# Kernel optimization log

Hardware: AMD Instinct MI355X
Metric: run time of the kernel (lower is better)

The kernel has to match this reference:

```python
import jax, jax.numpy as jnp
import numpy as np

B, T, D = 4, 1024, 1024
H = 16
DH = D // H            # head dim (attention_dim/num_heads)
FF = 4096
EPS = 1e-6             # allennlp LayerNorm eps
NEG = jnp.finfo(jnp.float32).min


def _layer_norm(x, g, b):
    # allennlp LayerNorm: (x - mean) / (unbiased_std + eps) * gamma + beta
    mean = jnp.mean(x, axis=-1, keepdims=True)
    var = jnp.var(x, axis=-1, keepdims=True) * (x.shape[-1] / (x.shape[-1] - 1))
    return g * (x - mean) / (jnp.sqrt(var) + EPS) + b


def setup_inputs() -> dict:
    key = jax.random.key(0)
    ks = jax.random.split(key, 12)
    s = lambda fan_in: 1.0 / np.sqrt(fan_in)
    return {
        "src": jax.random.normal(ks[0], (B, T, D), jnp.float32),
        "src_mask": jnp.ones((B, T), jnp.int32),
        # weights stored [in, out]
        "q_w": jax.random.uniform(ks[1], (D, D), jnp.float32, -s(D), s(D)),
        "q_b": jnp.zeros((D,), jnp.float32),
        "kv_w": jax.random.uniform(ks[2], (D, 2 * D), jnp.float32, -s(D), s(D)),
        "kv_b": jnp.zeros((2 * D,), jnp.float32),
        "out_w": jax.random.uniform(ks[3], (D, D), jnp.float32, -s(D), s(D)),
        "out_b": jnp.zeros((D,), jnp.float32),
        "ffn_w1": jax.random.uniform(ks[4], (D, FF), jnp.float32, -s(D), s(D)),
        "ffn_b1": jnp.zeros((FF,), jnp.float32),
        "ffn_w2": jax.random.uniform(ks[5], (FF, D), jnp.float32, -s(FF), s(FF)),
        "ffn_b2": jnp.zeros((D,), jnp.float32),
        "norm1_g": jnp.ones((D,), jnp.float32),
        "norm1_b": jnp.zeros((D,), jnp.float32),
        "norm2_g": jnp.ones((D,), jnp.float32),
        "norm2_b": jnp.zeros((D,), jnp.float32),
    }


def reference(src, src_mask, q_w, q_b, kv_w, kv_b, out_w, out_b,
              ffn_w1, ffn_b1, ffn_w2, ffn_b2,
              norm1_g, norm1_b, norm2_g, norm2_b):
    b, t, d = src.shape
    scale = jnp.asarray(DH ** 0.5, src.dtype)

    q = (src @ q_w + q_b).reshape(b, t, H, DH)
    kv = src @ kv_w + kv_b                         # (b,t,2D): first half keys, second half values
    k = kv[..., :D].reshape(b, t, H, DH)
    v = kv[..., D:].reshape(b, t, H, DH)

    # scaled dot-product: queries divided by sqrt(head_dim) before bmm
    logits = jnp.einsum("bqhd,bkhd->bhqk", q / scale, k)
    # memory_efficient masked_softmax: masked key positions -> dtype min
    mask = src_mask[:, None, None, :].astype(bool)  # (b,1,1,t) over keys
    logits = jnp.where(mask, logits, NEG)
    attn = jax.nn.softmax(logits, axis=-1)          # dropout off (eval)

    ctx = jnp.einsum("bhqk,bkhd->bqhd", attn, v).reshape(b, t, D)
    attn_out = ctx @ out_w + out_b

    out1 = _layer_norm(src + attn_out, norm1_g, norm1_b)
    ffn = jax.nn.relu(out1 @ ffn_w1 + ffn_b1) @ ffn_w2 + ffn_b2
    out2 = _layer_norm(out1 + ffn, norm2_g, norm2_b)
    return out2
```

## Files before the change

kernel.cpp:

```cpp
#include <hip/hip_runtime.h>

#define DEV __device__ __forceinline__
#define SB0 __builtin_amdgcn_sched_barrier(0)

typedef unsigned short u16;
typedef __attribute__((ext_vector_type(4))) float f32x4;
typedef __attribute__((ext_vector_type(8))) short short8;

DEV u16 f2bf(float f) {
  union { float f; unsigned u; } c; c.f = f;
  unsigned u = c.u;
  unsigned r = (u + 0x7FFFu + ((u >> 16) & 1u)) >> 16;
  return (u16)r;
}
DEV float bf2f(u16 h) {
  union { unsigned u; float f; } c; c.u = ((unsigned)h) << 16;
  return c.f;
}

DEV void gload16(const void* g, void* l) {
  __builtin_amdgcn_global_load_lds(
      (__attribute__((address_space(1))) void*)(g),
      (__attribute__((address_space(3))) void*)(l), 16, 0, 0);
}
DEV void vmc8() { asm volatile("s_waitcnt vmcnt(8)" ::: "memory"); SB0; }
DEV void vmc0() { asm volatile("s_waitcnt vmcnt(0)" ::: "memory"); SB0; }

__global__ __launch_bounds__(256) void prep_kernel(
    const float* __restrict__ src, const float* __restrict__ q_w,
    const float* __restrict__ kv_w, const float* __restrict__ out_w,
    const float* __restrict__ w1, const float* __restrict__ w2,
    u16* __restrict__ Xbf, u16* __restrict__ WqkvT, u16* __restrict__ WoT,
    u16* __restrict__ W1T, u16* __restrict__ W2T) {
  __shared__ float tile[32 * 33];
  int bb = blockIdx.x, tid = threadIdx.x;
  if (bb < 4096) {
    int i = bb * 256 + tid;
    float4 v = reinterpret_cast<const float4*>(src)[i];
    ushort4 o;
    o.x = f2bf(v.x); o.y = f2bf(v.y); o.z = f2bf(v.z); o.w = f2bf(v.w);
    reinterpret_cast<ushort4*>(Xbf)[i] = o;
    return;
  }
  const float* in; u16* outp; int ld_in, ld_out, bx, by;
  if (bb < 5120)       { int t = bb - 4096;  in = q_w;   outp = WqkvT; ld_in = 1024; ld_out = 1024; bx = t & 31;  by = t >> 5; }
  else if (bb < 7168)  { int t = bb - 5120;  in = kv_w;  outp = WqkvT + (size_t)1024 * 1024; ld_in = 2048; ld_out = 1024; bx = t & 63;  by = t >> 6; }
  else if (bb < 8192)  { int t = bb - 7168;  in = out_w; outp = WoT;   ld_in = 1024; ld_out = 1024; bx = t & 31;  by = t >> 5; }
  else if (bb < 12288) { int t = bb - 8192;  in = w1;    outp = W1T;   ld_in = 4096; ld_out = 1024; bx = t & 127; by = t >> 7; }
  else                 { int t = bb - 12288; in = w2;    outp = W2T;   ld_in = 1024; ld_out = 4096; bx = t & 31;  by = t >> 5; }
  int tx = tid & 31, ty = tid >> 5;
  int c0 = bx * 32, r0 = by * 32;
#pragma unroll
  for (int j = 0; j < 4; ++j)
    tile[(ty + j * 8) * 33 + tx] = in[(size_t)(r0 + ty + j * 8) * ld_in + c0 + tx];
  __syncthreads();
#pragma unroll
  for (int j = 0; j < 4; ++j)
    outp[(size_t)(c0 + ty + j * 8) * ld_out + r0 + tx] = f2bf(tile[tx * 33 + ty + j * 8]);
}

__global__ __launch_bounds__(256) void transpose_u16_kernel(
    const u16* __restrict__ in, int ld_in, int col_off,
    u16* __restrict__ out, int ld_out) {
  __shared__ float tile[32][33];
  int c0 = blockIdx.x * 32, r0 = blockIdx.y * 32;
  int tx = threadIdx.x, ty = threadIdx.y;
#pragma unroll
  for (int j = 0; j < 4; ++j) {
    int r = r0 + ty + j * 8;
    tile[ty + j * 8][tx] = bf2f(in[(size_t)r * ld_in + col_off + c0 + tx]);
  }
  __syncthreads();
#pragma unroll
  for (int j = 0; j < 4; ++j)
    out[(size_t)(c0 + ty + j * 8) * ld_out + r0 + tx] = f2bf(tile[tx][ty + j * 8]);
}

template <int BM, int NWARP, typename OutT, bool RELU>
__global__ __launch_bounds__(NWARP * 64, 2) void gemm_ring_kernel(
    const u16* __restrict__ A, int lda,
    const u16* __restrict__ Bt, int ldb,
    const float* __restrict__ bias, const float* __restrict__ bias2, int split,
    OutT* __restrict__ C, int ldc, int K, float scale) {
  constexpr int MT = BM / 32;
  constexpr int PWR = BM / 2;
  constexpr int WN = NWARP / 2;
  constexpr int SLOT = 2 * BM * 32;
  __shared__ __align__(16) u16 ring[4][SLOT];

  const int tid = threadIdx.x;
  const int lane = tid & 63, wid = tid >> 6;
  const int wr = wid / WN, wc = wid % WN;
  const int lr = lane & 15, hi = lane >> 4;

  const int gx = gridDim.x;
  const int nwg = gx * gridDim.y;
  const int orig = blockIdx.y * gx + blockIdx.x;
  const int q = nwg >> 3, r8 = nwg & 7, xcd = orig & 7, oo = orig >> 3;
  const int lid = (xcd < r8 ? xcd * (q + 1) : r8 * (q + 1) + (xcd - r8) * q) + oo;
  const int rb = lid / gx, cb = lid % gx;

  const u16* Abase = A + (size_t)rb * BM * lda;
  const u16* Bbase = Bt + (size_t)cb * BM * ldb;

  auto stage = [&](int slot, int kt) {
#pragma unroll
    for (int j = 0; j < 2; ++j) {
      int ch = wid * 2 + j;
      int row = ch * 16 + (lane >> 2);
      int cs = (lane & 3) ^ ((row >> 1) & 3);
      gload16(Abase + (size_t)row * lda + kt * 32 + cs * 8, &ring[slot][ch * 512]);
      gload16(Bbase + (size_t)row * ldb + kt * 32 + cs * 8, &ring[slot][BM * 32 + ch * 512]);
    }
  };

  f32x4 acc[MT][4];
  const f32x4 zero = {0.f, 0.f, 0.f, 0.f};
#pragma unroll
  for (int m = 0; m < MT; ++m)
#pragma unroll
    for (int n = 0; n < 4; ++n) acc[m][n] = zero;

  const int NT = K >> 5;
  stage(0, 0); stage(1, 1); stage(2, 2);
  vmc8();
  __builtin_amdgcn_s_barrier(); SB0;

  const int sw = (lr >> 1) & 3;
  for (int k = 0; k < NT; ++k) {
    const u16* la = &ring[k & 3][0];
    const u16* lb = &ring[k & 3][BM * 32];
    short8 bf[4], af[MT];
#pragma unroll
    for (int n = 0; n < 4; ++n)
      bf[n] = *(const short8*)(lb + (wc * 64 + n * 16 + lr) * 32 + ((hi ^ sw) * 8));
#pragma unroll
    for (int m = 0; m < MT; ++m)
      af[m] = *(const short8*)(la + (wr * PWR + m * 16 + lr) * 32 + ((hi ^ sw) * 8));
    if (k + 3 < NT) stage((k + 3) & 3, k + 3);
    __builtin_amdgcn_s_setprio(1);
#pragma unroll
    for (int m = 0; m < MT; ++m)
#pragma unroll
      for (int n = 0; n < 4; ++n)
        acc[m][n] = __builtin_amdgcn_mfma_f32_16x16x32_bf16(af[m], bf[n], acc[m][n], 0, 0, 0);
    __builtin_amdgcn_s_setprio(0);
    if (k + 4 < NT) vmc8();
    else if (k + 1 < NT) vmc0();
    __builtin_amdgcn_s_barrier(); SB0;
  }

#pragma unroll
  for (int m = 0; m < MT; ++m) {
    int row0 = rb * BM + wr * PWR + m * 16 + hi * 4;
#pragma unroll
    for (int n = 0; n < 4; ++n) {
      int col = cb * BM + wc * 64 + n * 16 + lr;
      float bv = 0.0f, sc = scale;
      if (col < split) bv = bias[col];
      else { bv = bias2[col - split]; sc = 1.0f; }
#pragma unroll
      for (int r = 0; r < 4; ++r) {
        float v = (acc[m][n][r] + bv) * sc;
        if (RELU) v = fmaxf(v, 0.0f);
        if constexpr (sizeof(OutT) == 2)
          C[(size_t)(row0 + r) * ldc + col] = f2bf(v);
        else
          C[(size_t)(row0 + r) * ldc + col] = v;
      }
    }
  }
}

__global__ __launch_bounds__(256) void attn_kernel(
    const u16* __restrict__ QKV, const u16* __restrict__ Vt,
    const int* __restrict__ mask, u16* __restrict__ CTX) {
  __shared__ __align__(16) u16 kl[2][64 * 64];
  __shared__ __align__(16) u16 vl[2][64 * 64];
  __shared__ __align__(16) u16 pl[4][32 * 64];
  const int lane = threadIdx.x & 63;
  const int wid = threadIdx.x >> 6;
  const int lr = lane & 15, hi = lane >> 4;
  const int bh = blockIdx.x, qt = blockIdx.y;
  const int b = bh >> 4, h = bh & 15;

  short8 qf[2][2];
#pragma unroll
  for (int m = 0; m < 2; ++m)
#pragma unroll
    for (int ks = 0; ks < 2; ++ks) {
      size_t grow = (size_t)(b * 1024 + qt * 128 + wid * 32 + m * 16 + lr);
      qf[m][ks] = *(const short8*)(QKV + grow * 3072 + h * 64 + ks * 32 + hi * 8);
    }

  unsigned long long keepm = 0ull;
#pragma unroll
  for (int kt = 0; kt < 16; ++kt)
#pragma unroll
    for (int n = 0; n < 4; ++n)
      if (mask[b * 1024 + kt * 64 + n * 16 + lr] != 0)
        keepm |= (1ull << (kt * 4 + n));

  const u16* Kbase = QKV + (size_t)(b * 1024) * 3072 + 1024 + h * 64;
  const u16* Vbase = Vt + (size_t)(h * 64) * 4096 + b * 1024;
  const int sr = lane >> 3;
  const int sc = lane & 7;

  auto stage = [&](int bf, int kt) {
#pragma unroll
    for (int j = 0; j < 2; ++j) {
      int r = wid * 16 + j * 8 + sr;
      int cs = sc ^ (r & 7);
      gload16(Kbase + (size_t)(kt * 64 + r) * 3072 + cs * 8,
              &kl[bf][(wid * 16 + j * 8) * 64]);
      gload16(Vbase + (size_t)r * 4096 + kt * 64 + cs * 8,
              &vl[bf][(wid * 16 + j * 8) * 64]);
    }
  };

  float m_run[2][4], l_run[2][4];
  f32x4 O[2][4];
  const f32x4 zero = {0.f, 0.f, 0.f, 0.f};
#pragma unroll
  for (int m = 0; m < 2; ++m) {
#pragma unroll
    for (int r = 0; r < 4; ++r) { m_run[m][r] = -3.0e38f; l_run[m][r] = 0.f; }
#pragma unroll
    for (int d = 0; d < 4; ++d) O[m][d] = zero;
  }

  stage(0, 0);
  __syncthreads();
  int cur = 0;
  for (int kt = 0; kt < 16; ++kt) {
    if (kt + 1 < 16) stage(cur ^ 1, kt + 1);

    short8 kf[4][2];
#pragma unroll
    for (int n = 0; n < 4; ++n) {
      int key = n * 16 + lr;
#pragma unroll
      for (int ks = 0; ks < 2; ++ks) {
        int ch = (hi + 4 * ks) ^ (key & 7);
        kf[n][ks] = *(const short8*)(kl[cur] + key * 64 + ch * 8);
      }
    }
    f32x4 s[2][4];
#pragma unroll
    for (int m = 0; m < 2; ++m)
#pragma unroll
      for (int n = 0; n < 4; ++n) s[m][n] = zero;
#pragma unroll
    for (int ks = 0; ks < 2; ++ks)
#pragma unroll
      for (int m = 0; m < 2; ++m)
#pragma unroll
        for (int n = 0; n < 4; ++n)
          s[m][n] = __builtin_amdgcn_mfma_f32_16x16x32_bf16(qf[m][ks], kf[n][ks], s[m][n], 0, 0, 0);

    bool keep[4];
#pragma unroll
    for (int n = 0; n < 4; ++n)
      keep[n] = (keepm >> (kt * 4 + n)) & 1ull;

#pragma unroll
    for (int m = 0; m < 2; ++m) {
#pragma unroll
      for (int r = 0; r < 4; ++r) {
        float sv[4];
#pragma unroll
        for (int n = 0; n < 4; ++n) {
          float x = s[m][n][r];
          sv[n] = keep[n] ? x : -3.0e38f;
        }
        float tm = fmaxf(fmaxf(sv[0], sv[1]), fmaxf(sv[2], sv[3]));
        tm = fmaxf(tm, __shfl_xor(tm, 1));
        tm = fmaxf(tm, __shfl_xor(tm, 2));
        tm = fmaxf(tm, __shfl_xor(tm, 4));
        tm = fmaxf(tm, __shfl_xor(tm, 8));
        float mo = m_run[m][r];
        float mn = fmaxf(mo, tm);
        float alpha = __expf(mo - mn);
        m_run[m][r] = mn;
        int prow = m * 16 + hi * 4 + r;
        float ps = 0.f;
        u16 pb[4];
#pragma unroll
        for (int n = 0; n < 4; ++n) {
          float p = __expf(sv[n] - mn);
          ps += p;
          pb[n] = f2bf(p);
        }
        l_run[m][r] = l_run[m][r] * alpha + ps;
#pragma unroll
        for (int d = 0; d < 4; ++d) O[m][d][r] *= alpha;
#pragma unroll
        for (int n = 0; n < 4; ++n) {
          int col = n * 16 + lr;
          int ch = (col >> 3) ^ (prow & 7);
          pl[wid][prow * 64 + ch * 8 + (col & 7)] = pb[n];
        }
      }
    }

#pragma unroll
    for (int ks = 0; ks < 2; ++ks) {
      short8 pa[2], vf[4];
#pragma unroll
      for (int m = 0; m < 2; ++m) {
        int prow = m * 16 + lr;
        int ch = (hi + 4 * ks) ^ (prow & 7);
        pa[m] = *(const short8*)(pl[wid] + prow * 64 + ch * 8);
      }
#pragma unroll
      for (int d = 0; d < 4; ++d) {
        int vrow = d * 16 + lr;
        int ch = (hi + 4 * ks) ^ (vrow & 7);
        vf[d] = *(const short8*)(vl[cur] + vrow * 64 + ch * 8);
      }
#pragma unroll
      for (int m = 0; m < 2; ++m)
#pragma unroll
        for (int d = 0; d < 4; ++d)
          O[m][d] = __builtin_amdgcn_mfma_f32_16x16x32_bf16(pa[m], vf[d], O[m][d], 0, 0, 0);
    }
    __syncthreads();
    cur ^= 1;
  }

#pragma unroll
  for (int m = 0; m < 2; ++m) {
#pragma unroll
    for (int r = 0; r < 4; ++r) {
      float l = l_run[m][r];
      l += __shfl_xor(l, 1);
      l += __shfl_xor(l, 2);
      l += __shfl_xor(l, 4);
      l += __shfl_xor(l, 8);
      float inv = 1.0f / l;
      size_t row = (size_t)(b * 1024 + qt * 128 + wid * 32 + m * 16 + hi * 4 + r);
#pragma unroll
      for (int d = 0; d < 4; ++d)
        CTX[row * 1024 + h * 64 + d * 16 + lr] = f2bf(O[m][d][r] * inv);
    }
  }
}

__global__ __launch_bounds__(256) void ln_kernel(
    const float* __restrict__ xa, const float* __restrict__ xb,
    const float* __restrict__ xc,
    const float* __restrict__ g, const float* __restrict__ beta,
    float* __restrict__ of, u16* __restrict__ ob) {
  int row = blockIdx.x;
  int tid = threadIdx.x;
  const float* pa = xa + (size_t)row * 1024;
  const float* pb = xb + (size_t)row * 1024;
  const float* pc = xc ? xc + (size_t)row * 1024 : nullptr;
  float v[4];
  float s = 0.f, s2 = 0.f;
#pragma unroll
  for (int j = 0; j < 4; ++j) {
    int c = tid + j * 256;
    float x = pa[c] + pb[c];
    if (pc) x += pc[c];
    v[j] = x; s += x; s2 += x * x;
  }
#pragma unroll
  for (int d = 1; d < 64; d <<= 1) {
    s += __shfl_xor(s, d);
    s2 += __shfl_xor(s2, d);
  }
  __shared__ float red[8];
  int w = tid >> 6, lane = tid & 63;
  if (lane == 0) { red[w] = s; red[4 + w] = s2; }
  __syncthreads();
  s = red[0] + red[1] + red[2] + red[3];
  s2 = red[4] + red[5] + red[6] + red[7];
  float mean = s * (1.0f / 1024.0f);
  float var = fmaxf((s2 - 1024.0f * mean * mean) * (1.0f / 1023.0f), 0.0f);
  float rden = 1.0f / (sqrtf(var) + 1e-6f);
#pragma unroll
  for (int j = 0; j < 4; ++j) {
    int c = tid + j * 256;
    float y = g[c] * (v[j] - mean) * rden + beta[c];
    of[(size_t)row * 1024 + c] = y;
    if (ob) ob[(size_t)row * 1024 + c] = f2bf(y);
  }
}

extern "C" void kernel_launch(void* const* d_in, const int* in_sizes, int n_in,
                              void* d_out, int out_size, void* d_ws, size_t ws_size,
                              hipStream_t stream) {
  const float* src   = (const float*)d_in[0];
  const int*   mask  = (const int*)d_in[1];
  const float* q_w   = (const float*)d_in[2];
  const float* q_b   = (const float*)d_in[3];
  const float* kv_w  = (const float*)d_in[4];
  const float* kv_b  = (const float*)d_in[5];
  const float* out_w = (const float*)d_in[6];
  const float* out_b = (const float*)d_in[7];
  const float* w1    = (const float*)d_in[8];
  const float* b1    = (const float*)d_in[9];
  const float* w2    = (const float*)d_in[10];
  const float* b2    = (const float*)d_in[11];
  const float* g1    = (const float*)d_in[12];
  const float* be1   = (const float*)d_in[13];
  const float* g2    = (const float*)d_in[14];
  const float* be2   = (const float*)d_in[15];
  float* out = (float*)d_out;

  char* ws = (char*)d_ws;
  const size_t MB = 1024 * 1024;
  const int BIG = 1 << 30;
  u16*  Xbf   = (u16*)(ws + 0);
  u16*  CTX   = (u16*)(ws + 8 * MB);
  u16*  WqkvT = (u16*)(ws + 16 * MB);
  u16*  WoT   = (u16*)(ws + 22 * MB);
  u16*  W1T   = (u16*)(ws + 24 * MB);
  u16*  W2T   = (u16*)(ws + 32 * MB);
  u16*  QKV   = (u16*)(ws + 40 * MB);
  u16*  Vt    = (u16*)(ws + 64 * MB);
  u16*  F1b   = (u16*)(ws + 40 * MB);
  float* AOUT = (float*)(ws + 72 * MB);
  float* OUT1F= (float*)(ws + 88 * MB);
  u16*  OUT1B = (u16*)(ws + 104 * MB);
  float* F2F  = (float*)(ws + 72 * MB);

  prep_kernel<<<dim3(16384), dim3(256), 0, stream>>>(
      src, q_w, kv_w, out_w, w1, w2, Xbf, WqkvT, WoT, W1T, W2T);
  gemm_ring_kernel<256, 8, u16, false><<<dim3(12, 16), dim3(512), 0, stream>>>(
      Xbf, 1024, WqkvT, 1024, q_b, kv_b, 1024, QKV, 3072, 1024, 0.125f);
  transpose_u16_kernel<<<dim3(32, 128), dim3(32, 8), 0, stream>>>(QKV, 3072, 2048, Vt, 4096);
  attn_kernel<<<dim3(64, 8), dim3(256), 0, stream>>>(QKV, Vt, mask, CTX);
  gemm_ring_kernel<128, 4, float, false><<<dim3(8, 32), dim3(256), 0, stream>>>(
      CTX, 1024, WoT, 1024, out_b, nullptr, BIG, AOUT, 1024, 1024, 1.0f);
  ln_kernel<<<dim3(4096), dim3(256), 0, stream>>>(src, AOUT, nullptr, g1, be1, OUT1F, OUT1B);
  gemm_ring_kernel<256, 8, u16, true><<<dim3(16, 16), dim3(512), 0, stream>>>(
      OUT1B, 1024, W1T, 1024, b1, nullptr, BIG, F1b, 4096, 1024, 1.0f);
  gemm_ring_kernel<128, 4, float, false><<<dim3(8, 32), dim3(256), 0, stream>>>(
      F1b, 4096, W2T, 4096, b2, nullptr, BIG, F2F, 1024, 4096, 1.0f);
  ln_kernel<<<dim3(4096), dim3(256), 0, stream>>>(OUT1F, F2F, nullptr, g2, be2, out, nullptr);
  (void)in_sizes; (void)n_in; (void)out_size; (void)ws_size;
}
```

Measured before the change: 347.2 us.

## Compute transposed S in attention to keep P in registers, drop LDS round-trip

New measurement: 316.6 us. 1.1x faster.

```diff
diff --git a/kernel.cpp b/kernel.cpp
--- a/kernel.cpp
+++ b/kernel.cpp
@@ -16,6 +16,11 @@
 DEV float bf2f(u16 h) {
   union { unsigned u; float f; } c; c.u = ((unsigned)h) << 16;
   return c.f;
+}
+DEV unsigned cvtpk(float a, float b) {
+  unsigned r;
+  asm("v_cvt_pk_bf16_f32 %0, %1, %2" : "=v"(r) : "v"(a), "v"(b));
+  return r;
 }
 
 DEV void gload16(const void* g, void* l) {
@@ -59,21 +64,22 @@
     outp[(size_t)(c0 + ty + j * 8) * ld_out + r0 + tx] = f2bf(tile[tx * 33 + ty + j * 8]);
 }
 
-__global__ __launch_bounds__(256) void transpose_u16_kernel(
-    const u16* __restrict__ in, int ld_in, int col_off,
-    u16* __restrict__ out, int ld_out) {
+__global__ __launch_bounds__(256) void transpose_vtp_kernel(
+    const u16* __restrict__ in, u16* __restrict__ out) {
   __shared__ float tile[32][33];
   int c0 = blockIdx.x * 32, r0 = blockIdx.y * 32;
   int tx = threadIdx.x, ty = threadIdx.y;
 #pragma unroll
-  for (int j = 0; j < 4; ++j) {
-    int r = r0 + ty + j * 8;
-    tile[ty + j * 8][tx] = bf2f(in[(size_t)r * ld_in + col_off + c0 + tx]);
-  }
+  for (int j = 0; j < 4; ++j)
+    tile[ty + j * 8][tx] = bf2f(in[(size_t)(r0 + ty + j * 8) * 3072 + 2048 + c0 + tx]);
   __syncthreads();
+  int k = r0 + tx;
+  int base = k & ~63, kb = k & 63;
+  int n = kb >> 4, w = kb & 15;
+  int p = ((n >> 1) << 5) | ((w >> 2) << 3) | ((n & 1) << 2) | (w & 3);
 #pragma unroll
   for (int j = 0; j < 4; ++j)
-    out[(size_t)(c0 + ty + j * 8) * ld_out + r0 + tx] = f2bf(tile[tx][ty + j * 8]);
+    out[(size_t)(c0 + ty + j * 8) * 4096 + base + p] = f2bf(tile[tx][ty + j * 8]);
 }
 
 template <int BM, int NWARP, typename OutT, bool RELU>
@@ -172,62 +178,46 @@
   }
 }
 
-__global__ __launch_bounds__(256) void attn_kernel(
-    const u16* __restrict__ QKV, const u16* __restrict__ Vt,
+__global__ __launch_bounds__(512, 2) void attn_kernel(
+    const u16* __restrict__ QKV, const u16* __restrict__ Vtp,
     const int* __restrict__ mask, u16* __restrict__ CTX) {
   __shared__ __align__(16) u16 kl[2][64 * 64];
   __shared__ __align__(16) u16 vl[2][64 * 64];
-  __shared__ __align__(16) u16 pl[4][32 * 64];
+  __shared__ unsigned long long mask_lds[16];
   const int lane = threadIdx.x & 63;
   const int wid = threadIdx.x >> 6;
   const int lr = lane & 15, hi = lane >> 4;
   const int bh = blockIdx.x, qt = blockIdx.y;
   const int b = bh >> 4, h = bh & 15;
 
-  short8 qf[2][2];
-#pragma unroll
-  for (int m = 0; m < 2; ++m)
-#pragma unroll
-    for (int ks = 0; ks < 2; ++ks) {
-      size_t grow = (size_t)(b * 1024 + qt * 128 + wid * 32 + m * 16 + lr);
-      qf[m][ks] = *(const short8*)(QKV + grow * 3072 + h * 64 + ks * 32 + hi * 8);
-    }
-
-  unsigned long long keepm = 0ull;
-#pragma unroll
-  for (int kt = 0; kt < 16; ++kt)
-#pragma unroll
-    for (int n = 0; n < 4; ++n)
-      if (mask[b * 1024 + kt * 64 + n * 16 + lr] != 0)
-        keepm |= (1ull << (kt * 4 + n));
+  const size_t qrow = (size_t)(b * 1024 + qt * 128 + wid * 16 + lr);
+  short8 qf[2];
+#pragma unroll
+  for (int ks = 0; ks < 2; ++ks)
+    qf[ks] = *(const short8*)(QKV + qrow * 3072 + h * 64 + ks * 32 + hi * 8);
+
+#pragma unroll
+  for (int i = 0; i < 2; ++i) {
+    int kt = wid * 2 + i;
+    unsigned long long bal = __ballot(mask[b * 1024 + kt * 64 + lane] != 0);
+    if (lane == 0) mask_lds[kt] = bal;
+  }
 
   const u16* Kbase = QKV + (size_t)(b * 1024) * 3072 + 1024 + h * 64;
-  const u16* Vbase = Vt + (size_t)(h * 64) * 4096 + b * 1024;
-  const int sr = lane >> 3;
-  const int sc = lane & 7;
+  const u16* Vbase = Vtp + (size_t)(h * 64) * 4096 + b * 1024;
 
   auto stage = [&](int bf, int kt) {
-#pragma unroll
-    for (int j = 0; j < 2; ++j) {
-      int r = wid * 16 + j * 8 + sr;
-      int cs = sc ^ (r & 7);
-      gload16(Kbase + (size_t)(kt * 64 + r) * 3072 + cs * 8,
-              &kl[bf][(wid * 16 + j * 8) * 64]);
-      gload16(Vbase + (size_t)r * 4096 + kt * 64 + cs * 8,
-              &vl[bf][(wid * 16 + j * 8) * 64]);
-    }
+    int r = wid * 8 + (lane >> 3);
+    int cs = (lane & 7) ^ (r & 7);
+    gload16(Kbase + (size_t)(kt * 64 + r) * 3072 + cs * 8, &kl[bf][wid * 8 * 64]);
+    gload16(Vbase + (size_t)r * 4096 + kt * 64 + cs * 8, &vl[bf][wid * 8 * 64]);
   };
 
-  float m_run[2][4], l_run[2][4];
-  f32x4 O[2][4];
+  float m_run = -3.0e38f, l_run = 0.0f;
+  f32x4 O[4];
   const f32x4 zero = {0.f, 0.f, 0.f, 0.f};
 #pragma unroll
-  for (int m = 0; m < 2; ++m) {
-#pragma unroll
-    for (int r = 0; r < 4; ++r) { m_run[m][r] = -3.0e38f; l_run[m][r] = 0.f; }
-#pragma unroll
-    for (int d = 0; d < 4; ++d) O[m][d] = zero;
-  }
+  for (int d = 0; d < 4; ++d) O[d] = zero;
 
   stage(0, 0);
   __syncthreads();
@@ -235,114 +225,93 @@
   for (int kt = 0; kt < 16; ++kt) {
     if (kt + 1 < 16) stage(cur ^ 1, kt + 1);
 
-    short8 kf[4][2];
+    f32x4 s[4];
+#pragma unroll
+    for (int n = 0; n < 4; ++n) s[n] = zero;
+    __builtin_amdgcn_s_setprio(1);
 #pragma unroll
     for (int n = 0; n < 4; ++n) {
       int key = n * 16 + lr;
 #pragma unroll
       for (int ks = 0; ks < 2; ++ks) {
         int ch = (hi + 4 * ks) ^ (key & 7);
-        kf[n][ks] = *(const short8*)(kl[cur] + key * 64 + ch * 8);
+        short8 kf = *(const short8*)(kl[cur] + key * 64 + ch * 8);
+        s[n] = __builtin_amdgcn_mfma_f32_16x16x32_bf16(kf, qf[ks], s[n], 0, 0, 0);
       }
     }
-    f32x4 s[2][4];
-#pragma unroll
-    for (int m = 0; m < 2; ++m)
-#pragma unroll
-      for (int n = 0; n < 4; ++n) s[m][n] = zero;
-#pragma unroll
-    for (int ks = 0; ks < 2; ++ks)
-#pragma unroll
-      for (int m = 0; m < 2; ++m)
-#pragma unroll
-        for (int n = 0; n < 4; ++n)
-          s[m][n] = __builtin_amdgcn_mfma_f32_16x16x32_bf16(qf[m][ks], kf[n][ks], s[m][n], 0, 0, 0);
-
-    bool keep[4];
+    __builtin_amdgcn_s_setprio(0);
+
+    unsigned long long mk = mask_lds[kt];
+    if (mk != ~0ull) {
+#pragma unroll
+      for (int n = 0; n < 4; ++n)
+#pragma unroll
+        for (int r = 0; r < 4; ++r)
+          if (!((mk >> (n * 16 + hi * 4 + r)) & 1ull)) s[n][r] = -3.0e38f;
+    }
+
+    float tm = -3.0e38f;
 #pragma unroll
     for (int n = 0; n < 4; ++n)
-      keep[n] = (keepm >> (kt * 4 + n)) & 1ull;
-
-#pragma unroll
-    for (int m = 0; m < 2; ++m) {
+      tm = fmaxf(tm, fmaxf(fmaxf(s[n][0], s[n][1]), fmaxf(s[n][2], s[n][3])));
+    tm = fmaxf(tm, __shfl_xor(tm, 16));
+    tm = fmaxf(tm, __shfl_xor(tm, 32));
+
+    float mo = m_run;
+    bool grow = __any(tm > mo);
+    float mn = grow ? fmaxf(mo, tm) : mo;
+    m_run = mn;
+    float ps = 0.0f;
+#pragma unroll
+    for (int n = 0; n < 4; ++n)
 #pragma unroll
       for (int r = 0; r < 4; ++r) {
-        float sv[4];
-#pragma unroll
-        for (int n = 0; n < 4; ++n) {
-          float x = s[m][n][r];
-          sv[n] = keep[n] ? x : -3.0e38f;
-        }
-        float tm = fmaxf(fmaxf(sv[0], sv[1]), fmaxf(sv[2], sv[3]));
-        tm = fmaxf(tm, __shfl_xor(tm, 1));
-        tm = fmaxf(tm, __shfl_xor(tm, 2));
-        tm = fmaxf(tm, __shfl_xor(tm, 4));
-        tm = fmaxf(tm, __shfl_xor(tm, 8));
-        float mo = m_run[m][r];
-        float mn = fmaxf(mo, tm);
-        float alpha = __expf(mo - mn);
-        m_run[m][r] = mn;
-        int prow = m * 16 + hi * 4 + r;
-        float ps = 0.f;
-        u16 pb[4];
-#pragma unroll
-        for (int n = 0; n < 4; ++n) {
-          float p = __expf(sv[n] - mn);
-          ps += p;
-          pb[n] = f2bf(p);
-        }
-        l_run[m][r] = l_run[m][r] * alpha + ps;
-#pragma unroll
-        for (int d = 0; d < 4; ++d) O[m][d][r] *= alpha;
-#pragma unroll
-        for (int n = 0; n < 4; ++n) {
-          int col = n * 16 + lr;
-          int ch = (col >> 3) ^ (prow & 7);
-          pl[wid][prow * 64 + ch * 8 + (col & 7)] = pb[n];
-        }
+        float p = __expf(s[n][r] - mn);
+        s[n][r] = p;
+        ps += p;
       }
+    if (grow) {
+      float alpha = __expf(mo - mn);
+      l_run = l_run * alpha + ps;
+#pragma unroll
+      for (int d = 0; d < 4; ++d)
+#pragma unroll
+        for (int r = 0; r < 4; ++r) O[d][r] *= alpha;
+    } else {
+      l_run += ps;
     }
 
 #pragma unroll
     for (int ks = 0; ks < 2; ++ks) {
-      short8 pa[2], vf[4];
-#pragma unroll
-      for (int m = 0; m < 2; ++m) {
-        int prow = m * 16 + lr;
-        int ch = (hi + 4 * ks) ^ (prow & 7);
-        pa[m] = *(const short8*)(pl[wid] + prow * 64 + ch * 8);
-      }
+      union { unsigned u[4]; short8 s8; } pf;
+      pf.u[0] = cvtpk(s[2 * ks][0], s[2 * ks][1]);
+      pf.u[1] = cvtpk(s[2 * ks][2], s[2 * ks][3]);
+      pf.u[2] = cvtpk(s[2 * ks + 1][0], s[2 * ks + 1][1]);
+      pf.u[3] = cvtpk(s[2 * ks + 1][2], s[2 * ks + 1][3]);
+      __builtin_amdgcn_s_setprio(1);
 #pragma unroll
       for (int d = 0; d < 4; ++d) {
         int vrow = d * 16 + lr;
         int ch = (hi + 4 * ks) ^ (vrow & 7);
-        vf[d] = *(const short8*)(vl[cur] + vrow * 64 + ch * 8);
+        short8 vf = *(const short8*)(vl[cur] + vrow * 64 + ch * 8);
+        O[d] = __builtin_amdgcn_mfma_f32_16x16x32_bf16(vf, pf.s8, O[d], 0, 0, 0);
       }
-#pragma unroll
-      for (int m = 0; m < 2; ++m)
-#pragma unroll
-        for (int d = 0; d < 4; ++d)
-          O[m][d] = __builtin_amdgcn_mfma_f32_16x16x32_bf16(pa[m], vf[d], O[m][d], 0, 0, 0);
+      __builtin_amdgcn_s_setprio(0);
     }
     __syncthreads();
     cur ^= 1;
   }
 
-#pragma unroll
-  for (int m = 0; m < 2; ++m) {
-#pragma unroll
-    for (int r = 0; r < 4; ++r) {
-      float l = l_run[m][r];
-      l += __shfl_xor(l, 1);
-      l += __shfl_xor(l, 2);
-      l += __shfl_xor(l, 4);
-      l += __shfl_xor(l, 8);
-      float inv = 1.0f / l;
-      size_t row = (size_t)(b * 1024 + qt * 128 + wid * 32 + m * 16 + hi * 4 + r);
-#pragma unroll
-      for (int d = 0; d < 4; ++d)
-        CTX[row * 1024 + h * 64 + d * 16 + lr] = f2bf(O[m][d][r] * inv);
-    }
+  float l = l_run;
+  l += __shfl_xor(l, 16);
+  l += __shfl_xor(l, 32);
+  float inv = 1.0f / l;
+#pragma unroll
+  for (int dt = 0; dt < 4; ++dt) {
+    uint2 w;
+    w.x = cvtpk(O[dt][0] * inv, O[dt][1] * inv);
+    w.y = cvtpk(O[dt][2] * inv, O[dt][3] * inv);
+    *(uint2*)(CTX + qrow * 1024 + h * 64 + dt * 16 + hi * 4) = w;
   }
 }
 
@@ -419,7 +388,7 @@
   u16*  W1T   = (u16*)(ws + 24 * MB);
   u16*  W2T   = (u16*)(ws + 32 * MB);
   u16*  QKV   = (u16*)(ws + 40 * MB);
-  u16*  Vt    = (u16*)(ws + 64 * MB);
+  u16*  Vtp   = (u16*)(ws + 64 * MB);
   u16*  F1b   = (u16*)(ws + 40 * MB);
   float* AOUT = (float*)(ws + 72 * MB);
   float* OUT1F= (float*)(ws + 88 * MB);
@@ -430,8 +399,8 @@
       src, q_w, kv_w, out_w, w1, w2, Xbf, WqkvT, WoT, W1T, W2T);
   gemm_ring_kernel<256, 8, u16, false><<<dim3(12, 16), dim3(512), 0, stream>>>(
       Xbf, 1024, WqkvT, 1024, q_b, kv_b, 1024, QKV, 3072, 1024, 0.125f);
-  transpose_u16_kernel<<<dim3(32, 128), dim3(32, 8), 0, stream>>>(QKV, 3072, 2048, Vt, 4096);
-  attn_kernel<<<dim3(64, 8), dim3(256), 0, stream>>>(QKV, Vt, mask, CTX);
+  transpose_vtp_kernel<<<dim3(32, 128), dim3(32, 8), 0, stream>>>(QKV, Vtp);
+  attn_kernel<<<dim3(64, 8), dim3(512), 0, stream>>>(QKV, Vtp, mask, CTX);
   gemm_ring_kernel<128, 4, float, false><<<dim3(8, 32), dim3(256), 0, stream>>>(
       CTX, 1024, WoT, 1024, out_b, nullptr, BIG, AOUT, 1024, 1024, 1.0f);
   ln_kernel<<<dim3(4096), dim3(256), 0, stream>>>(src, AOUT, nullptr, g1, be1, OUT1F, OUT1B);
```
